# Optimization experiments

Hardware: AMD Instinct MI355X
Metric: run time of the kernel (lower is better)

## Reference

```python
import jax, jax.numpy as jnp
import numpy as np

B, H, L = 32, 512, 2          # batch, hidden_dim, n_rnn layers per tier
F0 = 128                      # top-tier frame count
UPS = (2, 8)                  # up-sampling factors for tiers 0 and 1
FRAMES = (F0, F0 * UPS[0], F0 * UPS[0] * UPS[1])


def setup_inputs() -> dict:
    key = jax.random.key(0)
    ks = iter(jax.random.split(key, 64))
    k = 1.0 / np.sqrt(H)
    u = lambda shape: jax.random.uniform(next(ks), shape, jnp.float32, -k, k)
    inp = {}
    for t in range(3):
        inp[f"x{t}"] = jax.random.normal(next(ks), (B, FRAMES[t], H), jnp.float32)
    for t in range(3):
        inp[f"Wih{t}"] = u((L, 4 * H, H))
        inp[f"Whh{t}"] = u((L, 4 * H, H))
        inp[f"bih{t}"] = u((L, 4 * H))
        inp[f"bhh{t}"] = u((L, 4 * H))
        inp[f"h0_{t}"] = jax.random.normal(next(ks), (L, B, H), jnp.float32)
        inp[f"c0_{t}"] = jax.random.normal(next(ks), (L, B, H), jnp.float32)
    inp["upW0"] = u((H, UPS[0] * H)); inp["upb0"] = u((UPS[0] * H,))
    inp["upW1"] = u((H, UPS[1] * H)); inp["upb1"] = u((UPS[1] * H,))
    return inp


def _lstm(x, Wih, Whh, bih, bhh, h0, c0):
    # x: (B,T,H); Wih/Whh: (L,4H,H); torch gate order i,f,g,o
    for l in range(L):
        xg = jnp.einsum('bth,gh->btg', x, Wih[l]) + bih[l]  # (B,T,4H)
        Whh_l, bhh_l = Whh[l], bhh[l]

        def step(carry, g_t):
            h, c = carry
            g = g_t + h @ Whh_l.T + bhh_l
            i, f, gg, o = jnp.split(g, 4, axis=-1)
            c = jax.nn.sigmoid(f) * c + jax.nn.sigmoid(i) * jnp.tanh(gg)
            h = jax.nn.sigmoid(o) * jnp.tanh(c)
            return (h, c), h

        _, hs = jax.lax.scan(step, (h0[l], c0[l]), jnp.swapaxes(xg, 0, 1))
        x = jnp.swapaxes(hs, 0, 1)
    return x


def _upsample(x, W, b, t):
    # LinearResampler: Linear(H -> t*H) then unfold time: (B,T,H)->(B,T*t,H)
    Bx, T, Hx = x.shape
    y = x @ W + b  # (B,T,t*H)
    return y.reshape(Bx, T * t, Hx)


def reference(x0, x1, x2,
              Wih0, Whh0, bih0, bhh0, h0_0, c0_0,
              Wih1, Whh1, bih1, bhh1, h0_1, c0_1,
              Wih2, Whh2, bih2, bhh2, h0_2, c0_2,
              upW0, upb0, upW1, upb1):
    h = _lstm(x0, Wih0, Whh0, bih0, bhh0, h0_0, c0_0)
    h = _upsample(h, upW0, upb0, UPS[0])
    h = _lstm(x1 + h, Wih1, Whh1, bih1, bhh1, h0_1, c0_1)
    h = _upsample(h, upW1, upb1, UPS[1])
    h = _lstm(x2 + h, Wih2, Whh2, bih2, bhh2, h0_2, c0_2)
    return h
```

## Files before the change

kernel.cpp:

```cpp
#include <hip/hip_runtime.h>
#include <cstddef>
#include <cstdint>

#define NB 32
#define HD 512
#define GD 2048
#define NL0 32
#define NL1 64
#define NGB 160
#define FSTR 64
#define NSLOT 8
#define LOSC 0.00048828125f

typedef unsigned short u16;
typedef unsigned int u32;
typedef unsigned long long u64;
typedef _Float16 f16;
typedef __attribute__((ext_vector_type(8))) _Float16 f16x8;
typedef __attribute__((ext_vector_type(4))) float f32x4;

#define MFMAF(a, b, c) __builtin_amdgcn_mfma_f32_16x16x32_f16((a), (b), (c), 0, 0, 0)
#define AT_LD(p)   __hip_atomic_load((p), __ATOMIC_RELAXED, __HIP_MEMORY_SCOPE_AGENT)

#define LDG16(dst, p) \
    asm volatile("global_load_dwordx4 %0, %1, off sc0 sc1" : "=&v"(dst) : "v"(p))
#define ST8(p, v) \
    asm volatile("global_store_dwordx2 %0, %1, off sc0 sc1" :: "v"(p), "v"(v) : "memory")
#define VMCNT0() asm volatile("s_waitcnt vmcnt(0)" ::: "memory")
#define SBAR()   __builtin_amdgcn_sched_barrier(0)

__device__ __forceinline__ float sigf(float x)   { return 1.0f / (1.0f + __expf(-x)); }
__device__ __forceinline__ float tanhf_(float x) { return 2.0f / (1.0f + __expf(-2.0f * x)) - 1.0f; }

__device__ __forceinline__ u16 f2h_bits(float x) {
    f16 h = (f16)x; union { f16 f; u16 u; } c; c.f = h; return c.u;
}
__device__ __forceinline__ float h2f(u16 b) {
    union { u16 u; f16 f; } c; c.u = b; return (float)c.f;
}

__device__ __forceinline__ void split8f(const float4 a, const float4 b, f16x8& hi, f16x8& lo) {
    float v[8] = {a.x, a.y, a.z, a.w, b.x, b.y, b.z, b.w};
#pragma unroll
    for (int q = 0; q < 8; ++q) {
        const f16 h = (f16)v[q];
        hi[q] = h;
        lo[q] = (f16)((v[q] - (float)h) * 2048.0f);
    }
}
__device__ __forceinline__ void cvt8(const float4 a, const float4 b, f16x8& o) {
    o[0] = (f16)a.x; o[1] = (f16)a.y; o[2] = (f16)a.z; o[3] = (f16)a.w;
    o[4] = (f16)b.x; o[5] = (f16)b.y; o[6] = (f16)b.z; o[7] = (f16)b.w;
}

__global__ __launch_bounds__(256) void wsplit_kernel(
    const float* __restrict__ src, u16* __restrict__ hi, u16* __restrict__ lo, int n)
{
    const int i = blockIdx.x * 256 + threadIdx.x;
    if (i < n) {
        const float x = src[i];
        const f16 h = (f16)x;
        union { f16 f; u16 u; } c; c.f = h;
        hi[i] = c.u;
        lo[i] = f2h_bits((x - (float)h) * 2048.0f);
    }
}

__global__ __launch_bounds__(256) void cvtf_kernel(
    const float* __restrict__ src, u16* __restrict__ dst, int n)
{
    const int i = blockIdx.x * 256 + threadIdx.x;
    if (i < n) dst[i] = f2h_bits(src[i]);
}

__global__ __launch_bounds__(256) void addv_kernel(
    const float* __restrict__ a, const float* __restrict__ b, float* __restrict__ o, int n)
{
    const int i = blockIdx.x * 256 + threadIdx.x;
    if (i < n) o[i] = a[i] + b[i];
}

template<int MODE>
__global__ __launch_bounds__(256) void mfma_gemm(
    const float* __restrict__ A, int T, int t0, int tc_bits,
    const float* __restrict__ W, int N,
    const float* __restrict__ b1, const float* __restrict__ b2x,
    float* __restrict__ out, int t_bits, int u_bits)
{
    __shared__ __align__(16) u16 As[64][40], Bh[64][40], Bl[64][40];
    const int tid = threadIdx.x;
    const int m0 = blockIdx.x << 6, n0 = blockIdx.y << 6;

    const int ar = tid >> 2, aks = (tid & 3) << 3;
    const float* aPtr;
    if (MODE == 0) {
        const int rg = m0 + ar;
        const int b = rg >> tc_bits;
        const int tt = t0 + (rg & ((1 << tc_bits) - 1));
        aPtr = A + (((size_t)b * T + tt) << 9) + aks;
    } else {
        aPtr = A + (((size_t)(m0 + ar)) << 9) + aks;
    }
    const float* bPtr = nullptr;
    int bkk = 0, bns = 0;
    if (MODE == 0) {
        bPtr = W + (((size_t)(n0 + ar)) << 9) + aks;
    } else {
        bkk = tid >> 3; bns = (tid & 7) << 3;
        bPtr = W + (size_t)bkk * N + n0 + bns;
    }

    const int lane = tid & 63, wv = tid >> 6;
    const int fr = lane & 15, ko = (lane >> 4) << 3;
    f32x4 acc[4] = {}, accl[4] = {};

    for (int k0 = 0; k0 < HD; k0 += 32) {
        {
            const float4 a1 = *(const float4*)(aPtr + k0);
            const float4 a2 = *(const float4*)(aPtr + k0 + 4);
            f16x8 av; cvt8(a1, a2, av);
            *(f16x8*)&As[ar][aks] = av;
        }
        if (MODE == 0) {
            const float4 w1 = *(const float4*)(bPtr + k0);
            const float4 w2 = *(const float4*)(bPtr + k0 + 4);
            f16x8 vh, vl; split8f(w1, w2, vh, vl);
            *(f16x8*)&Bh[ar][aks] = vh;
            *(f16x8*)&Bl[ar][aks] = vl;
        } else {
            const float4 w1 = *(const float4*)(bPtr + (size_t)k0 * N);
            const float4 w2 = *(const float4*)(bPtr + (size_t)k0 * N + 4);
            f16x8 vh, vl; split8f(w1, w2, vh, vl);
#pragma unroll
            for (int q = 0; q < 8; ++q) {
                union { f16 f; u16 u; } ch, cl; ch.f = vh[q]; cl.f = vl[q];
                Bh[bns + q][bkk] = ch.u;
                Bl[bns + q][bkk] = cl.u;
            }
        }
        __syncthreads();
        const f16x8 ahf = *(const f16x8*)&As[(wv << 4) + fr][ko];
#pragma unroll
        for (int nt = 0; nt < 4; ++nt) {
            const f16x8 bhf = *(const f16x8*)&Bh[(nt << 4) + fr][ko];
            const f16x8 blf = *(const f16x8*)&Bl[(nt << 4) + fr][ko];
            acc[nt]  = MFMAF(ahf, bhf, acc[nt]);
            accl[nt] = MFMAF(ahf, blf, accl[nt]);
        }
        __syncthreads();
    }

    const int mlb = (wv << 4) + ((lane >> 4) << 2);
#pragma unroll
    for (int r = 0; r < 4; ++r) {
        const int mg = m0 + mlb + r;
#pragma unroll
        for (int nt = 0; nt < 4; ++nt) {
            const int n = n0 + (nt << 4) + fr;
            const float v = acc[nt][r] + accl[nt][r] * LOSC;
            if (MODE == 0) {
                out[((size_t)mg << 11) + n] = v + b1[n] + b2x[n];
            } else {
                const int bb = mg >> t_bits, tt = mg & ((1 << t_bits) - 1);
                const int uu = n >> 9, hh = n & 511;
                const size_t di = (((size_t)((((bb << t_bits) + tt) << u_bits) + uu)) << 9) + hh;
                out[di] = v + b1[n] + b2x[di];
            }
        }
    }
}


#define SPIN_WAIT(TGT0, TGT1) do { \
    if (tid < NL0 + NL1) { \
        const int tgt_ = (tid < NL0) ? (TGT0) : (TGT1); \
        if (tgt_ > 0) { \
            const u32* fp_ = flags + tid * FSTR; \
            int g_ = 0; \
            while ((int)AT_LD(fp_) < tgt_ && ++g_ < (1 << 24)) {} \
        } \
    } \
    SBAR(); \
    __syncthreads(); \
} while (0)

__global__ __launch_bounds__(512, 2) void lstm_scan8f(
    const float* __restrict__ xg, int Tc,
    const u16* __restrict__ w0h,
    const u16* __restrict__ w1ih_h,
    const u16* __restrict__ w1hh_h,
    const float* __restrict__ bsum1,
    u16* __restrict__ r0, u16* __restrict__ r1,
    float* __restrict__ c0ws, float* __restrict__ c1ws,
    float* __restrict__ out1, int T, int t0, int NS,
    u32* __restrict__ flags,
    const float* __restrict__ gA, int gt0, int gtc_bits,
    const float* __restrict__ gW,
    const float* __restrict__ gb1, const float* __restrict__ gb2x,
    float* __restrict__ gxg, int ntiles, int mtiles)
{
    __shared__ __align__(16) float sred[16 * 32 * 20];
    __shared__ u16 spk[16][33];
    __shared__ __align__(16) u16 gAs[64][40], gBh[64][40], gBl[64][40];
    const int tid = threadIdx.x;
    const int bid = blockIdx.x;
    const int lane = tid & 63, wv = tid >> 6;
    const int kq = wv >> 1, bh = wv & 1;
    const int fr = lane & 15, kg = lane >> 4;
    const int batch = (bh << 4) + fr;
    const int eb = tid & 31;
    const u32 bko = ((u32)batch << 9) + (kq << 7) + (kg << 3);

    if (bid < NL0) {
        const int j0 = bid << 4;
        f16x8 Ah_[16];
#pragma unroll
        for (int hq = 0; hq < 4; ++hq) {
            const size_t grow = (((size_t)(fr & 3)) << 9) + j0 + (hq << 2) + (fr >> 2);
#pragma unroll
            for (int ck = 0; ck < 4; ++ck)
                Ah_[(hq << 2) | ck] = *(const f16x8*)(
                    w0h + (grow << 9) + (kq << 7) + (ck << 5) + (kg << 3));
        }
        const int eh = tid >> 5;
        const int hidden = j0 + eh;
        float c_reg = c0ws[((size_t)eb << 9) + hidden];
        __syncthreads();

        for (int jj = 0; jj < Tc; ++jj) {
            const int t = t0 + jj;
            float xv[4];
#pragma unroll
            for (int g = 0; g < 4; ++g)
                xv[g] = xg[(((size_t)eb * Tc + jj) << 11) + (g << 9) + hidden];
            SPIN_WAIT(jj, jj - 6);
            const u16* bp = r0 + (((size_t)((t - 1) & 7)) << 14) + bko;
            f16x8 vb[4];
#pragma unroll
            for (int ck = 0; ck < 4; ++ck)
                LDG16(vb[ck], bp + (ck << 5));
            f32x4 s0[4] = {};
            VMCNT0(); SBAR();
#pragma unroll
            for (int hq = 0; hq < 4; ++hq)
#pragma unroll
                for (int ck = 0; ck < 4; ++ck)
                    s0[hq] = MFMAF(Ah_[(hq << 2) | ck], vb[ck], s0[hq]);
#pragma unroll
            for (int hq = 0; hq < 4; ++hq) {
                const int h16 = (hq << 2) + kg;
                *(f32x4*)&sred[((h16 << 5) + batch) * 20 + (kq << 2)] = s0[hq];
            }
            __syncthreads();
            {
                const int base = ((eh << 5) + eb) * 20;
                const f32x4 q0 = *(const f32x4*)&sred[base];
                const f32x4 q1 = *(const f32x4*)&sred[base + 4];
                const f32x4 q2 = *(const f32x4*)&sred[base + 8];
                const f32x4 q3 = *(const f32x4*)&sred[base + 12];
                const float gi = q0[0] + q1[0] + q2[0] + q3[0] + xv[0];
                const float gf = q0[1] + q1[1] + q2[1] + q3[1] + xv[1];
                const float gg = q0[2] + q1[2] + q2[2] + q3[2] + xv[2];
                const float go = q0[3] + q1[3] + q2[3] + q3[3] + xv[3];
                c_reg = sigf(gf) * c_reg + sigf(gi) * tanhf_(gg);
                const float h = sigf(go) * tanhf_(c_reg);
                spk[eh][eb] = f2h_bits(h);
            }
            __syncthreads();
            if (tid < 128) {
                const int bt = tid & 31, h4 = (tid >> 5) << 2;
                const u64 hp = (u64)spk[h4 + 0][bt] | ((u64)spk[h4 + 1][bt] << 16)
                             | ((u64)spk[h4 + 2][bt] << 32) | ((u64)spk[h4 + 3][bt] << 48);
                const size_t wo = (((size_t)(t & 7)) << 14) + ((size_t)bt << 9) + j0 + h4;
                ST8(r0 + wo, hp);
            }
            VMCNT0();
            __syncthreads();
            if (tid == 0)
                __hip_atomic_store(flags + bid * FSTR, (u32)(jj + 1),
                                   __ATOMIC_RELAXED, __HIP_MEMORY_SCOPE_AGENT);
        }
        c0ws[((size_t)eb << 9) + hidden] = c_reg;
    } else if (bid < NL0 + NL1) {
        const int j0 = (bid - NL0) << 3;
        f16x8 Ah_[16];
#pragma unroll
        for (int mat = 0; mat < 2; ++mat)
#pragma unroll
            for (int hq = 0; hq < 2; ++hq) {
                const size_t grow = (((size_t)(fr & 3)) << 9) + j0 + (hq << 2) + (fr >> 2);
                const u16* src = mat ? w1hh_h : w1ih_h;
#pragma unroll
                for (int ck = 0; ck < 4; ++ck)
                    Ah_[(((mat << 1) | hq) << 2) | ck] = *(const f16x8*)(
                        src + (grow << 9) + (kq << 7) + (ck << 5) + (kg << 3));
            }
        const int eh = tid >> 5;
        const int hidden = j0 + (eh & 7);
        float bs[4], c_reg = 0.f;
        if (tid < 256) {
#pragma unroll
            for (int g = 0; g < 4; ++g) bs[g] = bsum1[(g << 9) + hidden];
            c_reg = c1ws[((size_t)eb << 9) + hidden];
        }
        __syncthreads();

        for (int jj = 0; jj < NS; ++jj) {
            const int t = t0 + jj - 1;
            SPIN_WAIT(jj, jj);
            if (t >= 0) {
                const u16* ap = r0 + (((size_t)(t & 7)) << 14) + bko;
                const u16* bp = r1 + (((size_t)((t - 1) & 7)) << 14) + bko;
                f16x8 va[4], vb[4];
#pragma unroll
                for (int ck = 0; ck < 4; ++ck) {
                    LDG16(va[ck], ap + (ck << 5));
                    LDG16(vb[ck], bp + (ck << 5));
                }
                f32x4 s0[2] = {};
                VMCNT0(); SBAR();
#pragma unroll
                for (int hq = 0; hq < 2; ++hq)
#pragma unroll
                    for (int ck = 0; ck < 4; ++ck) {
                        const int ia = (hq << 2) | ck;
                        const int ib = ((2 + hq) << 2) | ck;
                        s0[hq] = MFMAF(Ah_[ia], va[ck], s0[hq]);
                        s0[hq] = MFMAF(Ah_[ib], vb[ck], s0[hq]);
                    }
#pragma unroll
                for (int hq = 0; hq < 2; ++hq) {
                    const int h8 = (hq << 2) + kg;
                    *(f32x4*)&sred[((h8 << 5) + batch) * 20 + (kq << 2)] = s0[hq];
                }
            }
            __syncthreads();
            if (t >= 0 && tid < 256) {
                const int base = ((eh << 5) + eb) * 20;
                const f32x4 q0 = *(const f32x4*)&sred[base];
                const f32x4 q1 = *(const f32x4*)&sred[base + 4];
                const f32x4 q2 = *(const f32x4*)&sred[base + 8];
                const f32x4 q3 = *(const f32x4*)&sred[base + 12];
                const float gi = q0[0] + q1[0] + q2[0] + q3[0] + bs[0];
                const float gf = q0[1] + q1[1] + q2[1] + q3[1] + bs[1];
                const float gg = q0[2] + q1[2] + q2[2] + q3[2] + bs[2];
                const float go = q0[3] + q1[3] + q2[3] + q3[3] + bs[3];
                c_reg = sigf(gf) * c_reg + sigf(gi) * tanhf_(gg);
                const float h = sigf(go) * tanhf_(c_reg);
                spk[eh][eb] = f2h_bits(h);
            }
            __syncthreads();
            if (t >= 0 && tid < 64) {
                const int bt = tid & 31, h4 = (tid >> 5) << 2;
                const u64 hp = (u64)spk[h4 + 0][bt] | ((u64)spk[h4 + 1][bt] << 16)
                             | ((u64)spk[h4 + 2][bt] << 32) | ((u64)spk[h4 + 3][bt] << 48);
                const size_t wo = (((size_t)(t & 7)) << 14) + ((size_t)bt << 9) + j0 + h4;
                ST8(r1 + wo, hp);
            }
            VMCNT0();
            __syncthreads();
            if (tid == 0)
                __hip_atomic_store(flags + (bid) * FSTR, (u32)(jj + 1),
                                   __ATOMIC_RELAXED, __HIP_MEMORY_SCOPE_AGENT);
            if (t >= 0 && tid < 64) {
                const int bt = tid & 31, h4 = (tid >> 5) << 2;
                float4 o;
                o.x = h2f(spk[h4 + 0][bt]);
                o.y = h2f(spk[h4 + 1][bt]);
                o.z = h2f(spk[h4 + 2][bt]);
                o.w = h2f(spk[h4 + 3][bt]);
                *(float4*)(out1 + (((size_t)bt * T + t) << 9) + j0 + h4) = o;
            }
        }
        if (tid < 256) c1ws[((size_t)eb << 9) + hidden] = c_reg;
    } else {
        const int gb = bid - (NL0 + NL1);
        const int ko = kg << 3;
        for (int tile = gb; tile < ntiles; tile += NGB) {
            const int m0 = (tile % mtiles) << 6;
            const int n0 = (tile / mtiles) << 6;
            const int ar = tid >> 2, aks = (tid & 3) << 3;
            const float* aPtr = nullptr;
            const float* bPtr = nullptr;
            if (tid < 256) {
                const int rg = m0 + ar;
                const int b = rg >> gtc_bits;
                const int tt = gt0 + (rg & ((1 << gtc_bits) - 1));
                aPtr = gA + (((size_t)b * T + tt) << 9) + aks;
                bPtr = gW + (((size_t)(n0 + ar)) << 9) + aks;
            }
            const int wv4 = (tid >> 6) & 3;
            f32x4 acc[4] = {}, accl[4] = {};
            for (int k0 = 0; k0 < HD; k0 += 32) {
                if (tid < 256) {
                    const float4 a1 = *(const float4*)(aPtr + k0);
                    const float4 a2 = *(const float4*)(aPtr + k0 + 4);
                    f16x8 av; cvt8(a1, a2, av);
                    *(f16x8*)&gAs[ar][aks] = av;
                    const float4 w1 = *(const float4*)(bPtr + k0);
                    const float4 w2 = *(const float4*)(bPtr + k0 + 4);
                    f16x8 vh, vl; split8f(w1, w2, vh, vl);
                    *(f16x8*)&gBh[ar][aks] = vh;
                    *(f16x8*)&gBl[ar][aks] = vl;
                }
                __syncthreads();
                if (tid < 256) {
                    const f16x8 ahf = *(const f16x8*)&gAs[(wv4 << 4) + fr][ko];
#pragma unroll
                    for (int nt = 0; nt < 4; ++nt) {
                        const f16x8 bhf = *(const f16x8*)&gBh[(nt << 4) + fr][ko];
                        const f16x8 blf = *(const f16x8*)&gBl[(nt << 4) + fr][ko];
                        acc[nt]  = MFMAF(ahf, bhf, acc[nt]);
                        accl[nt] = MFMAF(ahf, blf, accl[nt]);
                    }
                }
                __syncthreads();
            }
            if (tid < 256) {
                const int mlb = (wv4 << 4) + (kg << 2);
#pragma unroll
                for (int r = 0; r < 4; ++r) {
                    const int mg = m0 + mlb + r;
#pragma unroll
                    for (int nt = 0; nt < 4; ++nt) {
                        const int n = n0 + (nt << 4) + fr;
                        gxg[((size_t)mg << 11) + n] =
                            acc[nt][r] + accl[nt][r] * LOSC + gb1[n] + gb2x[n];
                    }
                }
            }
        }
    }
}

extern "C" void kernel_launch(void* const* d_in, const int* in_sizes, int n_in,
                              void* d_out, int out_size, void* d_ws, size_t ws_size,
                              hipStream_t stream)
{
    const float* x[3]   = {(const float*)d_in[0], (const float*)d_in[1],  (const float*)d_in[2]};
    const float* Wih[3] = {(const float*)d_in[3], (const float*)d_in[9],  (const float*)d_in[15]};
    const float* Whh[3] = {(const float*)d_in[4], (const float*)d_in[10], (const float*)d_in[16]};
    const float* bih[3] = {(const float*)d_in[5], (const float*)d_in[11], (const float*)d_in[17]};
    const float* bhh[3] = {(const float*)d_in[6], (const float*)d_in[12], (const float*)d_in[18]};
    const float* h0[3]  = {(const float*)d_in[7], (const float*)d_in[13], (const float*)d_in[19]};
    const float* c0[3]  = {(const float*)d_in[8], (const float*)d_in[14], (const float*)d_in[20]};
    const float* upW[2] = {(const float*)d_in[21], (const float*)d_in[23]};
    const float* upb[2] = {(const float*)d_in[22], (const float*)d_in[24]};

    float* ws = (float*)d_ws;
    float* bufA  = ws;
    float* bufB  = bufA + (size_t)NB * 256 * HD;
    float* c0ws  = bufB + (size_t)NB * 256 * HD;
    float* c1ws  = c0ws + (size_t)NB * HD;
    float* bsum1 = c1ws + (size_t)NB * HD;
    float* xgA   = bsum1 + GD;

    const size_t head_f = 2 * (size_t)NB * 256 * HD + 2 * (size_t)NB * HD + GD;
    const size_t tail_f = 3 * (size_t)GD * HD + NSLOT * (size_t)NB * HD + 96 * FSTR + 64;
    int Tc_cap = 512;
    while (Tc_cap > 32 && (head_f + 2 * (size_t)NB * Tc_cap * GD + tail_f) * 4 > ws_size)
        Tc_cap >>= 1;

    float* xgB  = xgA + (size_t)NB * Tc_cap * GD;
    u16* w0h    = (u16*)(xgB + (size_t)NB * Tc_cap * GD);
    u16* w0l    = w0h + (size_t)GD * HD;
    u16* w1ih_h = w0l + (size_t)GD * HD;
    u16* w1ih_l = w1ih_h + (size_t)GD * HD;
    u16* w1hh_h = w1ih_l + (size_t)GD * HD;
    u16* w1hh_l = w1hh_h + (size_t)GD * HD;
    u16* r0     = w1hh_l + (size_t)GD * HD;
    u16* r1     = r0 + NSLOT * (size_t)NB * HD;
    u32* flags  = (u32*)(r1 + NSLOT * (size_t)NB * HD);

    auto tier = [&](const float* in, float* out1, int T, int tr) {
        const float* Wih0L = Wih[tr];
        const float* Whh0L = Whh[tr];
        const float* Wih1L = Wih[tr] + (size_t)GD * HD;
        const float* Whh1L = Whh[tr] + (size_t)GD * HD;

        wsplit_kernel<<<(GD * HD) / 256, 256, 0, stream>>>(Whh0L, w0h, w0l, GD * HD);
        wsplit_kernel<<<(GD * HD) / 256, 256, 0, stream>>>(Wih1L, w1ih_h, w1ih_l, GD * HD);
        wsplit_kernel<<<(GD * HD) / 256, 256, 0, stream>>>(Whh1L, w1hh_h, w1hh_l, GD * HD);
        addv_kernel<<<GD / 256, 256, 0, stream>>>(bih[tr] + GD, bhh[tr] + GD, bsum1, GD);
        cvtf_kernel<<<(NB * HD) / 256, 256, 0, stream>>>(
            h0[tr], r0 + 7 * (size_t)NB * HD, NB * HD);
        cvtf_kernel<<<(NB * HD) / 256, 256, 0, stream>>>(
            h0[tr] + (size_t)NB * HD, r1 + 7 * (size_t)NB * HD, NB * HD);
        hipMemcpyAsync(c0ws, c0[tr], (size_t)NB * HD * sizeof(float),
                       hipMemcpyDeviceToDevice, stream);
        hipMemcpyAsync(c1ws, c0[tr] + (size_t)NB * HD, (size_t)NB * HD * sizeof(float),
                       hipMemcpyDeviceToDevice, stream);

        const int Tc = T < Tc_cap ? T : Tc_cap;
        int tc_bits = 0; while ((1 << tc_bits) < Tc) ++tc_bits;
        const int nchunks = T / Tc;
        const int mtiles = (NB * Tc) / 64;
        float* xgb[2] = {xgA, xgB};

        {
            dim3 g(mtiles, GD / 64);
            mfma_gemm<0><<<g, 256, 0, stream>>>(in, T, 0, tc_bits, Wih0L, GD,
                                                bih[tr], bhh[tr], xgb[0], 0, 0);
        }
        for (int ci = 0; ci < nchunks; ++ci) {
            const int t0 = ci * Tc;
            hipMemsetAsync(flags, 0, 96 * FSTR * sizeof(u32), stream);
            const bool last = (ci == nchunks - 1);
            const int NS = Tc + (last ? 1 : 0);
            const int ntiles = last ? 0 : mtiles * (GD / 64);
            const float* xg_p = xgb[ci & 1]; int Tc_a = Tc;
            const u16 *a0 = w0h, *a2 = w1ih_h, *a4 = w1hh_h;
            const float* bs_p = bsum1;
            u16 *p0 = r0, *p1 = r1;
            float *c0p = c0ws, *c1p = c1ws, *o1 = out1;
            int T_a = T, t0_a = t0, NS_a = NS;
            u32* fl = flags;
            const float* gA = in; int gt0 = t0 + Tc; int gtc = tc_bits;
            const float* gW = Wih0L; const float* g1 = bih[tr]; const float* g2 = bhh[tr];
            float* gx = xgb[(ci + 1) & 1]; int nt_a = ntiles; int mt_a = mtiles;
            void* args[] = {(void*)&xg_p, (void*)&Tc_a,
                            (void*)&a0, (void*)&a2, (void*)&a4,
                            (void*)&bs_p, (void*)&p0, (void*)&p1,
                            (void*)&c0p, (void*)&c1p, (void*)&o1,
                            (void*)&T_a, (void*)&t0_a, (void*)&NS_a, (void*)&fl,
                            (void*)&gA, (void*)&gt0, (void*)&gtc,
                            (void*)&gW, (void*)&g1, (void*)&g2,
                            (void*)&gx, (void*)&nt_a, (void*)&mt_a};
            hipLaunchCooperativeKernel((const void*)lstm_scan8f, dim3(256), dim3(512),
                                       args, 0, stream);
        }
    };

    float* dout = (float*)d_out;

    tier(x[0], bufB, 128, 0);
    {
        dim3 g((NB * 128) / 64, 1024 / 64);
        mfma_gemm<1><<<g, 256, 0, stream>>>(bufB, 0, 0, 0, upW[0], 1024,
                                            upb[0], x[1], bufA, 7, 1);
    }
    tier(bufA, bufB, 256, 1);
    {
        dim3 g((NB * 256) / 64, 4096 / 64);
        mfma_gemm<1><<<g, 256, 0, stream>>>(bufB, 0, 0, 0, upW[1], 4096,
                                            upb[1], x[2], dout, 8, 3);
    }
    tier(dout, dout, 2048, 2);
}
```

Before: 10.41 ms.

## Halve layer-1 LSTM blocks, giving each 16 hidden units and more GEMM blocks

Layer-1 recurrent blocks drop from 64 to 32, each now owning 16 hidden units with all 512 threads doing the gate epilogue. The freed blocks go to the overlapped next-chunk input GEMM (NGB 160 to 192), and the flag array and memset shrink to match. Each layer-1 block now holds twice as many f16 weight fragments in registers, so launch bounds drop to one block per CU. That raises register pressure and may lengthen the per-step critical path of layer 1.

```diff
diff --git a/kernel.cpp b/kernel.cpp
--- a/kernel.cpp
+++ b/kernel.cpp
@@ -6,8 +6,8 @@
 #define HD 512
 #define GD 2048
 #define NL0 32
-#define NL1 64
-#define NGB 160
+#define NL1 32
+#define NGB 192
 #define FSTR 64
 #define NSLOT 8
 #define LOSC 0.00048828125f
@@ -184,7 +184,7 @@
     __syncthreads(); \
 } while (0)
 
-__global__ __launch_bounds__(512, 2) void lstm_scan8f(
+__global__ __launch_bounds__(512, 1) void lstm_scan8g(
     const float* __restrict__ xg, int Tc,
     const u16* __restrict__ w0h,
     const u16* __restrict__ w1ih_h,
@@ -282,27 +282,24 @@
         }
         c0ws[((size_t)eb << 9) + hidden] = c_reg;
     } else if (bid < NL0 + NL1) {
-        const int j0 = (bid - NL0) << 3;
-        f16x8 Ah_[16];
-#pragma unroll
-        for (int mat = 0; mat < 2; ++mat)
-#pragma unroll
-            for (int hq = 0; hq < 2; ++hq) {
-                const size_t grow = (((size_t)(fr & 3)) << 9) + j0 + (hq << 2) + (fr >> 2);
-                const u16* src = mat ? w1hh_h : w1ih_h;
-#pragma unroll
-                for (int ck = 0; ck < 4; ++ck)
-                    Ah_[(((mat << 1) | hq) << 2) | ck] = *(const f16x8*)(
-                        src + (grow << 9) + (kq << 7) + (ck << 5) + (kg << 3));
-            }
+        const int j0 = (bid - NL0) << 4;
+        f16x8 Ai_[16], Ahh_[16];
+#pragma unroll
+        for (int hq = 0; hq < 4; ++hq) {
+            const size_t grow = (((size_t)(fr & 3)) << 9) + j0 + (hq << 2) + (fr >> 2);
+#pragma unroll
+            for (int ck = 0; ck < 4; ++ck) {
+                const size_t o = (grow << 9) + (kq << 7) + (ck << 5) + (kg << 3);
+                Ai_[(hq << 2) | ck]  = *(const f16x8*)(w1ih_h + o);
+                Ahh_[(hq << 2) | ck] = *(const f16x8*)(w1hh_h + o);
+            }
+        }
         const int eh = tid >> 5;
-        const int hidden = j0 + (eh & 7);
-        float bs[4], c_reg = 0.f;
-        if (tid < 256) {
-#pragma unroll
-            for (int g = 0; g < 4; ++g) bs[g] = bsum1[(g << 9) + hidden];
-            c_reg = c1ws[((size_t)eb << 9) + hidden];
-        }
+        const int hidden = j0 + eh;
+        float bs[4];
+#pragma unroll
+        for (int g = 0; g < 4; ++g) bs[g] = bsum1[(g << 9) + hidden];
+        float c_reg = c1ws[((size_t)eb << 9) + hidden];
         __syncthreads();
 
         for (int jj = 0; jj < NS; ++jj) {
@@ -317,25 +314,23 @@
                     LDG16(va[ck], ap + (ck << 5));
                     LDG16(vb[ck], bp + (ck << 5));
                 }
-                f32x4 s0[2] = {};
+                f32x4 s0[4] = {};
                 VMCNT0(); SBAR();
 #pragma unroll
-                for (int hq = 0; hq < 2; ++hq)
+                for (int hq = 0; hq < 4; ++hq)
 #pragma unroll
                     for (int ck = 0; ck < 4; ++ck) {
-                        const int ia = (hq << 2) | ck;
-                        const int ib = ((2 + hq) << 2) | ck;
-                        s0[hq] = MFMAF(Ah_[ia], va[ck], s0[hq]);
-                        s0[hq] = MFMAF(Ah_[ib], vb[ck], s0[hq]);
+                        s0[hq] = MFMAF(Ai_[(hq << 2) | ck], va[ck], s0[hq]);
+                        s0[hq] = MFMAF(Ahh_[(hq << 2) | ck], vb[ck], s0[hq]);
                     }
 #pragma unroll
-                for (int hq = 0; hq < 2; ++hq) {
-                    const int h8 = (hq << 2) + kg;
-                    *(f32x4*)&sred[((h8 << 5) + batch) * 20 + (kq << 2)] = s0[hq];
+                for (int hq = 0; hq < 4; ++hq) {
+                    const int h16 = (hq << 2) + kg;
+                    *(f32x4*)&sred[((h16 << 5) + batch) * 20 + (kq << 2)] = s0[hq];
                 }
             }
             __syncthreads();
-            if (t >= 0 && tid < 256) {
+            if (t >= 0) {
                 const int base = ((eh << 5) + eb) * 20;
                 const f32x4 q0 = *(const f32x4*)&sred[base];
                 const f32x4 q1 = *(const f32x4*)&sred[base + 4];
@@ -350,7 +345,7 @@
                 spk[eh][eb] = f2h_bits(h);
             }
             __syncthreads();
-            if (t >= 0 && tid < 64) {
+            if (t >= 0 && tid < 128) {
                 const int bt = tid & 31, h4 = (tid >> 5) << 2;
                 const u64 hp = (u64)spk[h4 + 0][bt] | ((u64)spk[h4 + 1][bt] << 16)
                              | ((u64)spk[h4 + 2][bt] << 32) | ((u64)spk[h4 + 3][bt] << 48);
@@ -360,9 +355,9 @@
             VMCNT0();
             __syncthreads();
             if (tid == 0)
-                __hip_atomic_store(flags + (bid) * FSTR, (u32)(jj + 1),
+                __hip_atomic_store(flags + bid * FSTR, (u32)(jj + 1),
                                    __ATOMIC_RELAXED, __HIP_MEMORY_SCOPE_AGENT);
-            if (t >= 0 && tid < 64) {
+            if (t >= 0 && tid < 128) {
                 const int bt = tid & 31, h4 = (tid >> 5) << 2;
                 float4 o;
                 o.x = h2f(spk[h4 + 0][bt]);
@@ -372,7 +367,7 @@
                 *(float4*)(out1 + (((size_t)bt * T + t) << 9) + j0 + h4) = o;
             }
         }
-        if (tid < 256) c1ws[((size_t)eb << 9) + hidden] = c_reg;
+        c1ws[((size_t)eb << 9) + hidden] = c_reg;
     } else {
         const int gb = bid - (NL0 + NL1);
         const int ko = kg << 3;
@@ -456,7 +451,7 @@
     float* xgA   = bsum1 + GD;
 
     const size_t head_f = 2 * (size_t)NB * 256 * HD + 2 * (size_t)NB * HD + GD;
-    const size_t tail_f = 3 * (size_t)GD * HD + NSLOT * (size_t)NB * HD + 96 * FSTR + 64;
+    const size_t tail_f = 3 * (size_t)GD * HD + NSLOT * (size_t)NB * HD + 64 * FSTR + 64;
     int Tc_cap = 512;
     while (Tc_cap > 32 && (head_f + 2 * (size_t)NB * Tc_cap * GD + tail_f) * 4 > ws_size)
         Tc_cap >>= 1;
@@ -504,7 +499,7 @@
         }
         for (int ci = 0; ci < nchunks; ++ci) {
             const int t0 = ci * Tc;
-            hipMemsetAsync(flags, 0, 96 * FSTR * sizeof(u32), stream);
+            hipMemsetAsync(flags, 0, 64 * FSTR * sizeof(u32), stream);
             const bool last = (ci == nchunks - 1);
             const int NS = Tc + (last ? 1 : 0);
             const int ntiles = last ? 0 : mtiles * (GD / 64);
@@ -526,7 +521,7 @@
                             (void*)&gA, (void*)&gt0, (void*)&gtc,
                             (void*)&gW, (void*)&g1, (void*)&g2,
                             (void*)&gx, (void*)&nt_a, (void*)&mt_a};
-            hipLaunchCooperativeKernel((const void*)lstm_scan8f, dim3(256), dim3(512),
+            hipLaunchCooperativeKernel((const void*)lstm_scan8g, dim3(256), dim3(512),
                                        args, 0, stream);
         }
     };
```

After: 10.77 ms. +3.5%, slower.
